# Optimization experiments

Measured on AMD Instinct MI355X. Metric: run time of the kernel, lower is better.

The kernel has to match this reference:

```python
import jax, jax.numpy as jnp
import numpy as np
from jax import lax

HID = 96              # hidden_dim (C)
DM  = 2 * HID         # SS2D d_model (real+imag interleaved channels)
DI  = 2 * DM          # d_inner (expand=2, VMamba default)
N   = 16              # d_state
K   = 4               # scan directions
R   = (DM + 15) // 16 # dt_rank = ceil(d_model/16)
B_, H_, W_ = 1, 64, 64


def _layernorm(x, w, b, eps=1e-5):
    m = x.mean(-1, keepdims=True)
    v = ((x - m) ** 2).mean(-1, keepdims=True)
    return (x - m) * lax.rsqrt(v + eps) * w + b


def _selective_scan(xs, delta, A, Bs, Cs):
    # xs, delta: (B,K,D,L); A: (K,D,N); Bs, Cs: (B,K,N,L)
    def step(h, inp):
        dt, Bt, Ct, ut = inp                              # (B,K,D),(B,K,N),(B,K,N),(B,K,D)
        dA = jnp.exp(dt[..., None] * A[None])             # (B,K,D,N)
        h = h * dA + dt[..., None] * Bt[:, :, None, :] * ut[..., None]
        y = jnp.einsum('bkdn,bkn->bkd', h, Ct)
        return h, y
    inputs = (jnp.moveaxis(delta, -1, 0), jnp.moveaxis(Bs, -1, 0),
              jnp.moveaxis(Cs, -1, 0), jnp.moveaxis(xs, -1, 0))
    h0 = jnp.zeros(xs.shape[:3] + (N,), xs.dtype)
    _, ys = lax.scan(step, h0, inputs)                    # (L,B,K,D)
    return jnp.moveaxis(ys, 0, -1)                        # (B,K,D,L)


def _forward_core(x, x_proj_w, dt_w, dt_b, A_logs, Ds):
    # x: (B, DI, H, W) -- 4-direction cross-scan (VMamba SS2D)
    B, D, H, W = x.shape
    L = H * W
    x_hw = x.reshape(B, D, L)
    x_wh = x.transpose(0, 1, 3, 2).reshape(B, D, L)
    x_hwwh = jnp.stack([x_hw, x_wh], axis=1)                    # (B,2,D,L)
    xs = jnp.concatenate([x_hwwh, jnp.flip(x_hwwh, -1)], 1)     # (B,4,D,L)
    x_dbl = jnp.einsum('bkdl,kcd->bkcl', xs, x_proj_w)          # (B,K,R+2N,L)
    dts, Bs, Cs = jnp.split(x_dbl, [R, R + N], axis=2)
    dts = jnp.einsum('bkrl,kdr->bkdl', dts, dt_w)
    delta = jax.nn.softplus(dts + dt_b[None, :, :, None])
    A = -jnp.exp(A_logs.reshape(K, D, N))
    ys = _selective_scan(xs, delta, A, Bs, Cs)
    out_y = ys + Ds.reshape(K, D)[None, :, :, None] * xs        # (B,4,D,L)
    inv_y = jnp.flip(out_y[:, 2:4], -1)
    tr = lambda t: t.reshape(B, D, W, H).transpose(0, 1, 3, 2).reshape(B, D, L)
    y = out_y[:, 0] + inv_y[:, 0] + tr(out_y[:, 1]) + tr(inv_y[:, 1])
    return y.transpose(0, 2, 1).reshape(B, H, W, D)


def _ss2d(x, in_proj_w, conv_w, conv_b, x_proj_w, dt_w, dt_b,
          A_logs, Ds, out_norm_w, out_norm_b, out_proj_w):
    # x: (B, H, Wf, DM)
    xz = x @ in_proj_w.T                                        # (B,H,Wf,2*DI)
    xc, z = jnp.split(xz, 2, axis=-1)
    xc = xc.transpose(0, 3, 1, 2)                               # (B,DI,H,Wf)
    xc = lax.conv_general_dilated(xc, conv_w, (1, 1), 'SAME',
                                  feature_group_count=DI,
                                  dimension_numbers=('NCHW', 'OIHW', 'NCHW'))
    xc = jax.nn.silu(xc + conv_b[None, :, None, None])
    y = _forward_core(xc, x_proj_w, dt_w, dt_b, A_logs, Ds)     # (B,H,Wf,DI)
    y = _layernorm(y, out_norm_w, out_norm_b)
    y = y * jax.nn.silu(z)
    return y @ out_proj_w.T                                     # (B,H,Wf,DM)


def _freq_vss(x, in_proj_w, conv_w, conv_b, x_proj_w, dt_w, dt_b,
              A_logs, Ds, out_norm_w, out_norm_b, out_proj_w):
    B, H, W, C = x.shape
    xf = jnp.fft.rfft2(x, axes=(1, 2), norm='ortho')            # (B,H,Wf,C) complex
    Wf = xf.shape[2]
    # interleave real/imag into channels: (B,H,Wf,C,2) -> (B,H,Wf,2C)
    x1 = jnp.stack([xf.real, xf.imag], axis=4).reshape(B, H, Wf, 2 * C)
    att = _ss2d(x1, in_proj_w, conv_w, conv_b, x_proj_w, dt_w, dt_b,
                A_logs, Ds, out_norm_w, out_norm_b, out_proj_w)
    att = att.reshape(B, H, Wf, C, 2)
    attc = lax.complex(att[..., 0], att[..., 1])
    x1r = jnp.fft.irfft2(attc, s=(H, W), axes=(1, 2), norm='ortho')
    return x + x1r                                              # residual (drop_path=0)


def setup_inputs() -> dict:
    key = jax.random.key(0)
    ks = jax.random.split(key, 8)
    s = 0.02
    return {
        'x': jax.random.normal(ks[0], (B_, H_, W_, HID), jnp.float32),
        'in_proj_w': jax.random.normal(ks[1], (2 * DI, DM), jnp.float32) * s,
        'conv_w': jax.random.normal(ks[2], (DI, 1, 3, 3), jnp.float32) * s,
        'conv_b': jnp.zeros((DI,), jnp.float32),
        'x_proj_w': jax.random.normal(ks[3], (K, R + 2 * N, DI), jnp.float32) * s,
        'dt_w': jax.random.normal(ks[4], (K, DI, R), jnp.float32) * s,
        'dt_b': jax.random.normal(ks[5], (K, DI), jnp.float32) * 0.1,
        'A_logs': jnp.tile(jnp.log(jnp.arange(1, N + 1, dtype=jnp.float32))[None], (K * DI, 1)),
        'Ds': jnp.ones((K * DI,), jnp.float32),
        'out_norm_w': jnp.ones((DI,), jnp.float32),
        'out_norm_b': jnp.zeros((DI,), jnp.float32),
        'out_proj_w': jax.random.normal(ks[6], (DM, DI), jnp.float32) * s,
    }


def reference(x, in_proj_w, conv_w, conv_b, x_proj_w, dt_w, dt_b,
              A_logs, Ds, out_norm_w, out_norm_b, out_proj_w):
    return _freq_vss(x, in_proj_w, conv_w, conv_b, x_proj_w, dt_w, dt_b,
                     A_logs, Ds, out_norm_w, out_norm_b, out_proj_w)
```

## Files before the change

### kernel.cpp

```cpp
#include <hip/hip_runtime.h>
#include <hip/hip_bf16.h>

#define LQ   2112
#define DQ   384
#define NST  16
#define HQ   64
#define WFQ  33
#define CQ   96
#define SC   33
#define KDN  24576

#define AIPW  0
#define ACW   147456
#define ACB   150912
#define AXPW  151296
#define ADTW  218880
#define ADTB  237312
#define AANEG 238848
#define ADS   263424
#define ANW   264960
#define ANB   265344
#define AOPW  265728
#define ARTOT 339456

#define OFF_FFT   339456
#define OFF_XZ    744960
#define OFF_XCV   2366976
#define OFF_G     3177984
#define OFF_SUMDT 3549696
#define OFF_HEND  3651072
#define OFF_YS    5273088

#define P_ZR  0
#define P_ZI  202752

static __device__ __forceinline__ float u2f(unsigned short u)
{ union { unsigned int i; float f; } v; v.i = ((unsigned int)u) << 16; return v.f; }

static __device__ __forceinline__ float ldin(const void* p, int o, int isbf)
{
    if (isbf) return u2f(((const unsigned short*)p)[o]);
    return ((const float*)p)[o];
}

static __device__ __forceinline__ int isbf_of(const void* ds)
{ return (((const unsigned int*)ds)[0] == 0x3F803F80u) ? 1 : 0; }

__global__ __launch_bounds__(256) void k_cvt_rfftw(
    const void* __restrict__ x,   const void* __restrict__ ipw,
    const void* __restrict__ cw,  const void* __restrict__ cb,
    const void* __restrict__ xpw, const void* __restrict__ dtw,
    const void* __restrict__ dtb, const void* __restrict__ alog,
    const void* __restrict__ ds,  const void* __restrict__ nw,
    const void* __restrict__ nb,  const void* __restrict__ opw,
    float* __restrict__ arena, float* __restrict__ Zr, float* __restrict__ Zi)
{
    const int isbf = isbf_of(ds);
    if (blockIdx.x < 1326) {
        int t = blockIdx.x * 256 + threadIdx.x;
        int o = t;
        if (o < 147456) { arena[t] = ldin(ipw, o, isbf); return; }  o -= 147456;
        if (o < 3456)   { arena[t] = ldin(cw, o, isbf);  return; }  o -= 3456;
        if (o < 384)    { arena[t] = ldin(cb, o, isbf);  return; }  o -= 384;
        if (o < 67584)  { arena[t] = ldin(xpw, o, isbf); return; }  o -= 67584;
        if (o < 18432)  { arena[t] = ldin(dtw, o, isbf); return; }  o -= 18432;
        if (o < 1536)   { arena[t] = ldin(dtb, o, isbf); return; }  o -= 1536;
        if (o < 24576)  { arena[t] = -expf(ldin(alog, o, isbf)); return; }  o -= 24576;
        if (o < 1536)   { arena[t] = ldin(ds, o, isbf);  return; }  o -= 1536;
        if (o < 384)    { arena[t] = ldin(nw, o, isbf);  return; }  o -= 384;
        if (o < 384)    { arena[t] = ldin(nb, o, isbf);  return; }  o -= 384;
        arena[t] = ldin(opw, o, isbf);
        return;
    }
    __shared__ float tc[64], ts[64];
    if (threadIdx.x < 64) {
        float ang = -6.283185307179586f * (float)threadIdx.x / 64.f;
        float s, c; __sincosf(ang, &s, &c); tc[threadIdx.x] = c; ts[threadIdx.x] = s;
    }
    __syncthreads();
    int tid = (blockIdx.x - 1326) * 256 + threadIdx.x;
    int c = tid % CQ; int f = (tid / CQ) % WFQ; int h = tid / (CQ * WFQ);
    const int base = h * 64 * CQ + c;
    float zr = 0.f, zi = 0.f; int j = 0;
#pragma unroll 4
    for (int w = 0; w < 64; w++) {
        float xv = ldin(x, base + w * CQ, isbf);
        zr += xv * tc[j]; zi += xv * ts[j];
        j += f; j &= 63;
    }
    Zr[tid] = zr; Zi[tid] = zi;
}

__global__ __launch_bounds__(256) void k_ffth(const float* __restrict__ Zr, const float* __restrict__ Zi,
                                              float* __restrict__ x1)
{
    __shared__ float tc[64], ts[64];
    if (threadIdx.x < 64) {
        float ang = -6.283185307179586f * (float)threadIdx.x / 64.f;
        float s, c; __sincosf(ang, &s, &c); tc[threadIdx.x] = c; ts[threadIdx.x] = s;
    }
    __syncthreads();
    int tid = blockIdx.x * 256 + threadIdx.x;
    int c = tid % CQ; int f = (tid / CQ) % WFQ; int u = tid / (CQ * WFQ);
    float xr = 0.f, xi = 0.f; int j = 0;
    int base = f * CQ + c;
#pragma unroll 4
    for (int h = 0; h < 64; h++) {
        float zr = Zr[base + h * (WFQ * CQ)];
        float zi = Zi[base + h * (WFQ * CQ)];
        xr += zr * tc[j] - zi * ts[j];
        xi += zr * ts[j] + zi * tc[j];
        j += u; j &= 63;
    }
    int l = u * WFQ + f;
    x1[l * 192 + 2 * c]     = xr * (1.f / 64.f);
    x1[l * 192 + 2 * c + 1] = xi * (1.f / 64.f);
}

typedef __attribute__((ext_vector_type(8))) __bf16 bf16x8;
typedef __attribute__((ext_vector_type(4))) float f32x4;

__global__ __launch_bounds__(256) void k_gemm(const float* __restrict__ A, const float* __restrict__ W,
                                              float* __restrict__ C, int N, int K, int sW, int sC)
{
    W += (size_t)blockIdx.z * sW; C += (size_t)blockIdx.z * sC;
    __shared__ __bf16 Asm[64 * 40];
    __shared__ __bf16 Bsm[64 * 40];
    const int tid = threadIdx.x;
    const int bm = blockIdx.y * 64, bn = blockIdx.x * 64;
    const int wv = tid >> 6, lane = tid & 63;
    const int srow = tid >> 2, skk = (tid & 3) * 8;
    const int fm = lane & 15, fq = lane >> 4;
    f32x4 acc0 = {0.f, 0.f, 0.f, 0.f}, acc1 = acc0, acc2 = acc0, acc3 = acc0;
    const __bf16* afp = Asm + (wv * 16 + fm) * 40 + fq * 8;
    const __bf16* bfp = Bsm + fm * 40 + fq * 8;
    for (int k0 = 0; k0 < K; k0 += 32) {
        {
            const float* ap = A + (size_t)(bm + srow) * K + k0 + skk;
            float4 a0 = *(const float4*)ap, a1 = *(const float4*)(ap + 4);
            bf16x8 v = { (__bf16)a0.x, (__bf16)a0.y, (__bf16)a0.z, (__bf16)a0.w,
                         (__bf16)a1.x, (__bf16)a1.y, (__bf16)a1.z, (__bf16)a1.w };
            *(bf16x8*)(Asm + srow * 40 + skk) = v;
        }
        {
            float4 b0 = {0.f,0.f,0.f,0.f}, b1 = b0;
            if (bn + srow < N) {
                const float* wp = W + (size_t)(bn + srow) * K + k0 + skk;
                b0 = *(const float4*)wp; b1 = *(const float4*)(wp + 4);
            }
            bf16x8 v = { (__bf16)b0.x, (__bf16)b0.y, (__bf16)b0.z, (__bf16)b0.w,
                         (__bf16)b1.x, (__bf16)b1.y, (__bf16)b1.z, (__bf16)b1.w };
            *(bf16x8*)(Bsm + srow * 40 + skk) = v;
        }
        __syncthreads();
        bf16x8 af = *(const bf16x8*)afp;
        bf16x8 fb0 = *(const bf16x8*)(bfp);
        bf16x8 fb1 = *(const bf16x8*)(bfp + 16 * 40);
        bf16x8 fb2 = *(const bf16x8*)(bfp + 32 * 40);
        bf16x8 fb3 = *(const bf16x8*)(bfp + 48 * 40);
        acc0 = __builtin_amdgcn_mfma_f32_16x16x32_bf16(af, fb0, acc0, 0, 0, 0);
        acc1 = __builtin_amdgcn_mfma_f32_16x16x32_bf16(af, fb1, acc1, 0, 0, 0);
        acc2 = __builtin_amdgcn_mfma_f32_16x16x32_bf16(af, fb2, acc2, 0, 0, 0);
        acc3 = __builtin_amdgcn_mfma_f32_16x16x32_bf16(af, fb3, acc3, 0, 0, 0);
        __syncthreads();
    }
    const int m0 = bm + wv * 16 + fq * 4;
#pragma unroll
    for (int nt = 0; nt < 4; nt++) {
        f32x4 a = (nt == 0) ? acc0 : ((nt == 1) ? acc1 : ((nt == 2) ? acc2 : acc3));
        int n = bn + nt * 16 + fm;
        if (n < N) {
#pragma unroll
            for (int r = 0; r < 4; r++)
                C[(size_t)(m0 + r) * N + n] = a[r];
        }
    }
}

__global__ __launch_bounds__(256) void k_conv(const float* __restrict__ xz,
                                              const float* __restrict__ ar,
                                              float* __restrict__ xcv)
{
    int tid = blockIdx.x * 256 + threadIdx.x;
    int d = tid % DQ; int lp = tid / DQ;
    int l0 = lp * 2;
    float w9[9];
#pragma unroll
    for (int i = 0; i < 9; i++) w9[i] = ar[ACW + d * 9 + i];
    float cb = ar[ACB + d];
#pragma unroll
    for (int q = 0; q < 2; q++) {
        int l = l0 + q;
        int h = l / WFQ; int f = l % WFQ;
        float acc = cb;
#pragma unroll
        for (int ky = 0; ky < 3; ky++) {
            int hh = h + ky - 1;
            if (hh < 0 || hh >= HQ) continue;
#pragma unroll
            for (int kx = 0; kx < 3; kx++) {
                int ff = f + kx - 1;
                if (ff < 0 || ff >= WFQ) continue;
                acc += w9[ky * 3 + kx] * xz[(size_t)(hh * WFQ + ff) * 768 + d];
            }
        }
        float sig = 1.f / (1.f + __expf(-acc));
        xcv[(size_t)l * DQ + d] = acc * sig;
    }
}

static __device__ __forceinline__ float softplus_f(float a)
{
    return (a > 15.f) ? a : __logf(1.f + __expf(a));
}

template<int KK> static __device__ __forceinline__ int chunk_l0(int s)
{
    if (KK == 0) return s * 64;
    if (KK == 1) return s;
    if (KK == 2) return 2111 - s * 64;
    return 2111 - s;
}
template<int KK> static __device__ __forceinline__ int chunk_stp()
{
    if (KK == 0) return 1;
    if (KK == 1) return 33;
    if (KK == 2) return -1;
    return -33;
}

template<int KK, int PASS2> static __device__ __forceinline__ void scan_body(
    const float* __restrict__ xcv, const float* __restrict__ G, const float* __restrict__ ar,
    float* __restrict__ hend, float* __restrict__ sumdt, float* __restrict__ ysum,
    float* __restrict__ dtL, float* __restrict__ duL)
{
    const int s = blockIdx.x, db = blockIdx.y;
    const int lane = threadIdx.x;
    const int d = lane & 15, ng = lane >> 4;
    const int stp = chunk_stp<KK>();
    const int l0 = chunk_l0<KK>(s);
    const float* Gk = G + (size_t)KK * (LQ * 44);

    {
        const int st = lane;
        const int lt = l0 + stp * st;
        const float* gr = Gk + lt * 44;
        float4 g0 = *(const float4*)(gr);
        float4 g1 = *(const float4*)(gr + 4);
        float4 g2 = *(const float4*)(gr + 8);
        const float* ub = xcv + (size_t)lt * DQ + db * 16;
        float uu[16];
        *(float4*)(uu)      = *(const float4*)(ub);
        *(float4*)(uu + 4)  = *(const float4*)(ub + 4);
        *(float4*)(uu + 8)  = *(const float4*)(ub + 8);
        *(float4*)(uu + 12) = *(const float4*)(ub + 12);
#pragma unroll
        for (int j = 0; j < 16; j++) {
            const int kdj = KK * DQ + db * 16 + j;
            const float* wp = ar + ADTW + kdj * 12;
            float acc = ar[ADTB + kdj]
                + wp[0] * g0.x + wp[1] * g0.y + wp[2]  * g0.z + wp[3]  * g0.w
                + wp[4] * g1.x + wp[5] * g1.y + wp[6]  * g1.z + wp[7]  * g1.w
                + wp[8] * g2.x + wp[9] * g2.y + wp[10] * g2.z + wp[11] * g2.w;
            float dtv = softplus_f(acc);
            dtL[st * 17 + j] = dtv;
            duL[st * 17 + j] = dtv * uu[j];
        }
    }
    if (!PASS2 && KK == 0) {
        float4 z4 = make_float4(0.f, 0.f, 0.f, 0.f);
        float* zp = ysum + (size_t)(l0 + lane) * DQ + db * 16;
        *(float4*)zp = z4; *(float4*)(zp + 4) = z4;
        *(float4*)(zp + 8) = z4; *(float4*)(zp + 12) = z4;
    }
    __syncthreads();

    const int kd = KK * DQ + db * 16 + d;
    const int kdn = kd * NST + 4 * ng;
    const float4 Av = *(const float4*)(ar + AANEG + kdn);
    float h0 = 0.f, h1 = 0.f, h2 = 0.f, h3 = 0.f;
    if (PASS2) {
        float4 hh = *(const float4*)(hend + (size_t)s * KDN + kdn);
        h0 = hh.x; h1 = hh.y; h2 = hh.z; h3 = hh.w;
    }

#pragma unroll 8
    for (int i = 0; i < 64; i++) {
        const int l = l0 + stp * i;
        float dt = dtL[i * 17 + d];
        float du = duL[i * 17 + d];
        float4 bv = *(const float4*)(Gk + l * 44 + 12 + 4 * ng);
        h0 = h0 * __expf(dt * Av.x) + du * bv.x;
        h1 = h1 * __expf(dt * Av.y) + du * bv.y;
        h2 = h2 * __expf(dt * Av.z) + du * bv.z;
        h3 = h3 * __expf(dt * Av.w) + du * bv.w;
        if (PASS2) {
            float4 cv = *(const float4*)(Gk + l * 44 + 28 + 4 * ng);
            float yp = h0 * cv.x + h1 * cv.y + h2 * cv.z + h3 * cv.w;
            yp += __shfl_xor(yp, 16);
            yp += __shfl_xor(yp, 32);
            if (ng == 0) atomicAdd(&ysum[(size_t)l * DQ + db * 16 + d], yp);
        }
    }

    if (!PASS2) {
        *(float4*)(hend + (size_t)s * KDN + kdn) = make_float4(h0, h1, h2, h3);
        float sd = 0.f;
#pragma unroll
        for (int t = 0; t < 16; t++) sd += dtL[(ng * 16 + t) * 17 + d];
        sd += __shfl_xor(sd, 16);
        sd += __shfl_xor(sd, 32);
        if (ng == 0) sumdt[s * 1536 + kd] = sd;
    }
}

__global__ __launch_bounds__(64, 4) void k_scan1(const float* __restrict__ xcv, const float* __restrict__ G,
                                                 const float* __restrict__ ar,
                                                 float* __restrict__ hend, float* __restrict__ sumdt,
                                                 float* __restrict__ ysum)
{
    __shared__ float smem[2 * 64 * 17];
    float* dtL = smem; float* duL = smem + 64 * 17;
    switch (blockIdx.z) {
        case 0: scan_body<0, 0>(xcv, G, ar, hend, sumdt, ysum, dtL, duL); break;
        case 1: scan_body<1, 0>(xcv, G, ar, hend, sumdt, ysum, dtL, duL); break;
        case 2: scan_body<2, 0>(xcv, G, ar, hend, sumdt, ysum, dtL, duL); break;
        default: scan_body<3, 0>(xcv, G, ar, hend, sumdt, ysum, dtL, duL); break;
    }
}

__global__ __launch_bounds__(64, 4) void k_scan2(const float* __restrict__ xcv, const float* __restrict__ G,
                                                 const float* __restrict__ ar,
                                                 float* __restrict__ hend, float* __restrict__ sumdt,
                                                 float* __restrict__ ysum)
{
    __shared__ float smem[2 * 64 * 17];
    float* dtL = smem; float* duL = smem + 64 * 17;
    switch (blockIdx.z) {
        case 0: scan_body<0, 1>(xcv, G, ar, hend, sumdt, ysum, dtL, duL); break;
        case 1: scan_body<1, 1>(xcv, G, ar, hend, sumdt, ysum, dtL, duL); break;
        case 2: scan_body<2, 1>(xcv, G, ar, hend, sumdt, ysum, dtL, duL); break;
        default: scan_body<3, 1>(xcv, G, ar, hend, sumdt, ysum, dtL, duL); break;
    }
}

__global__ __launch_bounds__(256) void k_comb(const float* __restrict__ ar, const float* __restrict__ sumdt,
                                              float* __restrict__ hend)
{
    int tid = blockIdx.x * 256 + threadIdx.x;
    int kd = tid >> 4;
    float Av = ar[AANEG + tid];
    float hp = 0.f;
    for (int s = 0; s < SC; s++) {
        float he = hend[(size_t)s * KDN + tid];
        hend[(size_t)s * KDN + tid] = hp;
        hp = hp * __expf(Av * sumdt[s * 1536 + kd]) + he;
    }
}

__global__ __launch_bounds__(256) void k_lngemm(const float* __restrict__ ysum, const float* __restrict__ xcv,
                                                const float* __restrict__ xz, const float* __restrict__ ar,
                                                float* __restrict__ att)
{
    __shared__ __bf16 Asm[64 * 40];
    __shared__ __bf16 Bsm[64 * 40];
    __shared__ float rowm[64], rowr[64];
    __shared__ float sdk[DQ], nwk[DQ], nbk[DQ];
    const int tid = threadIdx.x;
    const int bm = blockIdx.y * 64, bn = blockIdx.x * 64;

    for (int k = tid; k < DQ; k += 256) {
        sdk[k] = ar[ADS + k] + ar[ADS + DQ + k] + ar[ADS + 2 * DQ + k] + ar[ADS + 3 * DQ + k];
        nwk[k] = ar[ANW + k];
        nbk[k] = ar[ANB + k];
    }
    __syncthreads();

    {
        const int r = tid >> 2, seg = tid & 3;
        const float* yp = ysum + (size_t)(bm + r) * DQ + seg * 96;
        const float* xp = xcv  + (size_t)(bm + r) * DQ + seg * 96;
        float s1 = 0.f, s2 = 0.f;
#pragma unroll 8
        for (int k = 0; k < 96; k += 4) {
            float4 yv = *(const float4*)(yp + k);
            float4 xv = *(const float4*)(xp + k);
            float4 sv = *(const float4*)(sdk + seg * 96 + k);
            float a0 = yv.x + sv.x * xv.x; float a1 = yv.y + sv.y * xv.y;
            float a2 = yv.z + sv.z * xv.z; float a3 = yv.w + sv.w * xv.w;
            s1 += a0 + a1 + a2 + a3;
            s2 += a0 * a0 + a1 * a1 + a2 * a2 + a3 * a3;
        }
        s1 += __shfl_xor(s1, 1); s2 += __shfl_xor(s2, 1);
        s1 += __shfl_xor(s1, 2); s2 += __shfl_xor(s2, 2);
        if (seg == 0) {
            float m = s1 * (1.f / 384.f);
            float var = s2 * (1.f / 384.f) - m * m;
            rowm[r] = m; rowr[r] = rsqrtf(var + 1e-5f);
        }
    }
    __syncthreads();

    const int wv = tid >> 6, lane = tid & 63;
    const int srow = tid >> 2, skk = (tid & 3) * 8;
    const int fm = lane & 15, fq = lane >> 4;
    f32x4 acc0 = {0.f, 0.f, 0.f, 0.f}, acc1 = acc0, acc2 = acc0, acc3 = acc0;
    const __bf16* afp = Asm + (wv * 16 + fm) * 40 + fq * 8;
    const __bf16* bfp = Bsm + fm * 40 + fq * 8;
    const float W_rm = rowm[srow], W_rr = rowr[srow];
    for (int k0 = 0; k0 < 384; k0 += 32) {
        {
            const size_t rb = (size_t)(bm + srow) * DQ + k0 + skk;
            float4 y0 = *(const float4*)(ysum + rb), y1 = *(const float4*)(ysum + rb + 4);
            float4 x0 = *(const float4*)(xcv + rb),  x1 = *(const float4*)(xcv + rb + 4);
            const float* zp = xz + (size_t)(bm + srow) * 768 + 384 + k0 + skk;
            float4 z0 = *(const float4*)(zp), z1 = *(const float4*)(zp + 4);
            float va[8];
            float ya[8] = { y0.x, y0.y, y0.z, y0.w, y1.x, y1.y, y1.z, y1.w };
            float xa[8] = { x0.x, x0.y, x0.z, x0.w, x1.x, x1.y, x1.z, x1.w };
            float za[8] = { z0.x, z0.y, z0.z, z0.w, z1.x, z1.y, z1.z, z1.w };
#pragma unroll
            for (int e = 0; e < 8; e++) {
                int k = k0 + skk + e;
                float a = ya[e] + sdk[k] * xa[e];
                float zn = za[e];
                float sig = 1.f / (1.f + __expf(-zn));
                va[e] = ((a - W_rm) * W_rr * nwk[k] + nbk[k]) * (zn * sig);
            }
            bf16x8 v = { (__bf16)va[0], (__bf16)va[1], (__bf16)va[2], (__bf16)va[3],
                         (__bf16)va[4], (__bf16)va[5], (__bf16)va[6], (__bf16)va[7] };
            *(bf16x8*)(Asm + srow * 40 + skk) = v;
        }
        {
            const float* wp = ar + AOPW + (size_t)(bn + srow) * 384 + k0 + skk;
            float4 b0 = *(const float4*)wp, b1 = *(const float4*)(wp + 4);
            bf16x8 v = { (__bf16)b0.x, (__bf16)b0.y, (__bf16)b0.z, (__bf16)b0.w,
                         (__bf16)b1.x, (__bf16)b1.y, (__bf16)b1.z, (__bf16)b1.w };
            *(bf16x8*)(Bsm + srow * 40 + skk) = v;
        }
        __syncthreads();
        bf16x8 af = *(const bf16x8*)afp;
        bf16x8 fb0 = *(const bf16x8*)(bfp);
        bf16x8 fb1 = *(const bf16x8*)(bfp + 16 * 40);
        bf16x8 fb2 = *(const bf16x8*)(bfp + 32 * 40);
        bf16x8 fb3 = *(const bf16x8*)(bfp + 48 * 40);
        acc0 = __builtin_amdgcn_mfma_f32_16x16x32_bf16(af, fb0, acc0, 0, 0, 0);
        acc1 = __builtin_amdgcn_mfma_f32_16x16x32_bf16(af, fb1, acc1, 0, 0, 0);
        acc2 = __builtin_amdgcn_mfma_f32_16x16x32_bf16(af, fb2, acc2, 0, 0, 0);
        acc3 = __builtin_amdgcn_mfma_f32_16x16x32_bf16(af, fb3, acc3, 0, 0, 0);
        __syncthreads();
    }
    const int m0 = bm + wv * 16 + fq * 4;
#pragma unroll
    for (int nt = 0; nt < 4; nt++) {
        f32x4 a = (nt == 0) ? acc0 : ((nt == 1) ? acc1 : ((nt == 2) ? acc2 : acc3));
        int n = bn + nt * 16 + fm;
#pragma unroll
        for (int r = 0; r < 4; r++)
            att[(size_t)(m0 + r) * 192 + n] = a[r];
    }
}

__global__ __launch_bounds__(256) void k_iffth(const float* __restrict__ att,
                                               float* __restrict__ Yr, float* __restrict__ Yi)
{
    __shared__ float tc[64], ts[64];
    if (threadIdx.x < 64) {
        float ang = 6.283185307179586f * (float)threadIdx.x / 64.f;
        float s, c; __sincosf(ang, &s, &c); tc[threadIdx.x] = c; ts[threadIdx.x] = s;
    }
    __syncthreads();
    int tid = blockIdx.x * 256 + threadIdx.x;
    int c = tid % CQ; int f = (tid / CQ) % WFQ; int hp = tid / (CQ * WFQ);
    float yr = 0.f, yi = 0.f; int j = 0;
#pragma unroll 4
    for (int h = 0; h < 64; h++) {
        const float* ap = att + (size_t)(h * WFQ + f) * 192 + 2 * c;
        float arv = ap[0], aiv = ap[1];
        yr += arv * tc[j] - aiv * ts[j];
        yi += arv * ts[j] + aiv * tc[j];
        j += hp; j &= 63;
    }
    Yr[tid] = yr * 0.125f;
    Yi[tid] = yi * 0.125f;
}

__global__ __launch_bounds__(256) void k_irfft_res(const float* __restrict__ Yr, const float* __restrict__ Yi,
                                                   const void* __restrict__ x, const void* __restrict__ ds,
                                                   void* __restrict__ out)
{
    __shared__ float tc[64], ts[64];
    if (threadIdx.x < 64) {
        float ang = 6.283185307179586f * (float)threadIdx.x / 64.f;
        float s, c; __sincosf(ang, &s, &c); tc[threadIdx.x] = c; ts[threadIdx.x] = s;
    }
    __syncthreads();
    const int isbf = isbf_of(ds);
    int tid = blockIdx.x * 256 + threadIdx.x;
    int c = tid % CQ; int w = (tid / CQ) % 64; int h = tid / (CQ * 64);
    const float* yr = Yr + h * (WFQ * CQ) + c;
    const float* yi = Yi + h * (WFQ * CQ) + c;
    float acc = yr[0];
    acc += ((w & 1) ? -1.f : 1.f) * yr[32 * CQ];
    float a2 = 0.f; int j = w & 63;
#pragma unroll 4
    for (int f = 1; f < 32; f++) {
        a2 += yr[f * CQ] * tc[j] - yi[f * CQ] * ts[j];
        j += w; j &= 63;
    }
    acc += 2.f * a2;
    float val = ldin(x, tid, isbf) + 0.125f * acc;
    if (isbf) ((__hip_bfloat16*)out)[tid] = __float2bfloat16(val);
    else      ((float*)out)[tid] = val;
}

extern "C" void kernel_launch(void* const* d_in, const int* in_sizes, int n_in,
                              void* d_out, int out_size, void* d_ws, size_t ws_size,
                              hipStream_t stream)
{
    float* ws    = (float*)d_ws;
    float* ar    = ws;
    float* Zr    = ws + OFF_FFT + P_ZR;
    float* Zi    = ws + OFF_FFT + P_ZI;
    float* xz    = ws + OFF_XZ;
    float* xcv   = ws + OFF_XCV;
    float* G     = ws + OFF_G;
    float* sumdt = ws + OFF_SUMDT;
    float* hend  = ws + OFF_HEND;
    float* YS    = ws + OFF_YS;

    float* x1   = YS;
    float* ysum = YS;
    float* att  = hend;

    k_cvt_rfftw<<<2118, 256, 0, stream>>>(d_in[0], d_in[1], d_in[2], d_in[3], d_in[4], d_in[5],
                                          d_in[6], d_in[7], d_in[8], d_in[9], d_in[10], d_in[11],
                                          ar, Zr, Zi);
    k_ffth<<<792, 256, 0, stream>>>(Zr, Zi, x1);
    k_gemm<<<dim3(12, 33, 1), 256, 0, stream>>>(x1, ar + AIPW, xz, 768, 192, 0, 0);
    k_conv<<<1584, 256, 0, stream>>>(xz, ar, xcv);
    k_gemm<<<dim3(1, 33, 4), 256, 0, stream>>>(xcv, ar + AXPW, G, 44, 384, 44 * 384, LQ * 44);
    k_scan1<<<dim3(SC, 24, 4), 64, 0, stream>>>(xcv, G, ar, hend, sumdt, ysum);
    k_comb<<<96, 256, 0, stream>>>(ar, sumdt, hend);
    k_scan2<<<dim3(SC, 24, 4), 64, 0, stream>>>(xcv, G, ar, hend, sumdt, ysum);
    k_lngemm<<<dim3(3, 33, 1), 256, 0, stream>>>(ysum, xcv, xz, ar, att);
    k_iffth<<<792, 256, 0, stream>>>(att, Zr, Zi);
    k_irfft_res<<<1536, 256, 0, stream>>>(Zr, Zi, d_in[0], d_in[8], d_out);
}
```

Before: 226.7 us.

## Halve scan chunk length, stage B/C in LDS, batch y atomics, prefetch combine

Doubles the number of scan chunks from 33 to 66 so each chunk covers 32 steps, giving more parallel blocks and a shorter serial loop per block. The per-step B and C vectors are staged once in shared memory instead of being reloaded from global memory every step. Per-step y atomics are buffered in LDS and flushed in one pass at the end. The chunk-combine kernel now software-prefetches hend and sumdt in groups of six. The cost is a longer sequential combine pass, larger hend and sumdt buffers, and more shared memory per block.

```diff
diff --git a/kernel.cpp b/kernel.cpp
--- a/kernel.cpp
+++ b/kernel.cpp
@@ -7,7 +7,7 @@
 #define HQ   64
 #define WFQ  33
 #define CQ   96
-#define SC   33
+#define SC   66
 #define KDN  24576
 
 #define AIPW  0
@@ -216,10 +216,10 @@
 
 template<int KK> static __device__ __forceinline__ int chunk_l0(int s)
 {
-    if (KK == 0) return s * 64;
-    if (KK == 1) return s;
-    if (KK == 2) return 2111 - s * 64;
-    return 2111 - s;
+    if (KK == 0) return s * 32;
+    if (KK == 1) return (s & 1) * 1056 + (s >> 1);
+    if (KK == 2) return 2111 - s * 32;
+    return 2111 - (s & 1) * 1056 - (s >> 1);
 }
 template<int KK> static __device__ __forceinline__ int chunk_stp()
 {
@@ -232,7 +232,8 @@
 template<int KK, int PASS2> static __device__ __forceinline__ void scan_body(
     const float* __restrict__ xcv, const float* __restrict__ G, const float* __restrict__ ar,
     float* __restrict__ hend, float* __restrict__ sumdt, float* __restrict__ ysum,
-    float* __restrict__ dtL, float* __restrict__ duL)
+    float* __restrict__ dtL, float* __restrict__ duL,
+    float* __restrict__ bvL, float* __restrict__ cvL, float* __restrict__ yL)
 {
     const int s = blockIdx.x, db = blockIdx.y;
     const int lane = threadIdx.x;
@@ -242,32 +243,42 @@
     const float* Gk = G + (size_t)KK * (LQ * 44);
 
     {
-        const int st = lane;
+        const int st = lane & 31;
+        const int hi = lane >> 5;
+        const int jb = hi * 8;
         const int lt = l0 + stp * st;
         const float* gr = Gk + lt * 44;
         float4 g0 = *(const float4*)(gr);
         float4 g1 = *(const float4*)(gr + 4);
         float4 g2 = *(const float4*)(gr + 8);
-        const float* ub = xcv + (size_t)lt * DQ + db * 16;
-        float uu[16];
-        *(float4*)(uu)      = *(const float4*)(ub);
-        *(float4*)(uu + 4)  = *(const float4*)(ub + 4);
-        *(float4*)(uu + 8)  = *(const float4*)(ub + 8);
-        *(float4*)(uu + 12) = *(const float4*)(ub + 12);
-#pragma unroll
-        for (int j = 0; j < 16; j++) {
-            const int kdj = KK * DQ + db * 16 + j;
+        float4 b0 = *(const float4*)(gr + 12 + jb);
+        float4 b1 = *(const float4*)(gr + 16 + jb);
+        *(float4*)(bvL + st * 20 + jb)     = b0;
+        *(float4*)(bvL + st * 20 + jb + 4) = b1;
+        if (PASS2) {
+            float4 c0 = *(const float4*)(gr + 28 + jb);
+            float4 c1 = *(const float4*)(gr + 32 + jb);
+            *(float4*)(cvL + st * 20 + jb)     = c0;
+            *(float4*)(cvL + st * 20 + jb + 4) = c1;
+        }
+        const float* ub = xcv + (size_t)lt * DQ + db * 16 + jb;
+        float uu[8];
+        *(float4*)(uu)     = *(const float4*)(ub);
+        *(float4*)(uu + 4) = *(const float4*)(ub + 4);
+#pragma unroll
+        for (int j = 0; j < 8; j++) {
+            const int kdj = KK * DQ + db * 16 + jb + j;
             const float* wp = ar + ADTW + kdj * 12;
             float acc = ar[ADTB + kdj]
                 + wp[0] * g0.x + wp[1] * g0.y + wp[2]  * g0.z + wp[3]  * g0.w
                 + wp[4] * g1.x + wp[5] * g1.y + wp[6]  * g1.z + wp[7]  * g1.w
                 + wp[8] * g2.x + wp[9] * g2.y + wp[10] * g2.z + wp[11] * g2.w;
             float dtv = softplus_f(acc);
-            dtL[st * 17 + j] = dtv;
-            duL[st * 17 + j] = dtv * uu[j];
-        }
-    }
-    if (!PASS2 && KK == 0) {
+            dtL[st * 17 + jb + j] = dtv;
+            duL[st * 17 + jb + j] = dtv * uu[j];
+        }
+    }
+    if (!PASS2 && KK == 0 && lane < 32) {
         float4 z4 = make_float4(0.f, 0.f, 0.f, 0.f);
         float* zp = ysum + (size_t)(l0 + lane) * DQ + db * 16;
         *(float4*)zp = z4; *(float4*)(zp + 4) = z4;
@@ -285,21 +296,20 @@
     }
 
 #pragma unroll 8
-    for (int i = 0; i < 64; i++) {
-        const int l = l0 + stp * i;
+    for (int i = 0; i < 32; i++) {
         float dt = dtL[i * 17 + d];
         float du = duL[i * 17 + d];
-        float4 bv = *(const float4*)(Gk + l * 44 + 12 + 4 * ng);
+        float4 bv = *(const float4*)(bvL + i * 20 + 4 * ng);
         h0 = h0 * __expf(dt * Av.x) + du * bv.x;
         h1 = h1 * __expf(dt * Av.y) + du * bv.y;
         h2 = h2 * __expf(dt * Av.z) + du * bv.z;
         h3 = h3 * __expf(dt * Av.w) + du * bv.w;
         if (PASS2) {
-            float4 cv = *(const float4*)(Gk + l * 44 + 28 + 4 * ng);
+            float4 cv = *(const float4*)(cvL + i * 20 + 4 * ng);
             float yp = h0 * cv.x + h1 * cv.y + h2 * cv.z + h3 * cv.w;
             yp += __shfl_xor(yp, 16);
             yp += __shfl_xor(yp, 32);
-            if (ng == 0) atomicAdd(&ysum[(size_t)l * DQ + db * 16 + d], yp);
+            if (ng == 0) yL[i * 17 + d] = yp;
         }
     }
 
@@ -307,10 +317,18 @@
         *(float4*)(hend + (size_t)s * KDN + kdn) = make_float4(h0, h1, h2, h3);
         float sd = 0.f;
 #pragma unroll
-        for (int t = 0; t < 16; t++) sd += dtL[(ng * 16 + t) * 17 + d];
+        for (int t = 0; t < 8; t++) sd += dtL[(ng * 8 + t) * 17 + d];
         sd += __shfl_xor(sd, 16);
         sd += __shfl_xor(sd, 32);
         if (ng == 0) sumdt[s * 1536 + kd] = sd;
+    } else {
+        __syncthreads();
+        const int wst = lane & 31, whi = lane >> 5;
+        const int wl = l0 + stp * wst;
+        float* yp = ysum + (size_t)wl * DQ + db * 16 + whi * 8;
+#pragma unroll
+        for (int e = 0; e < 8; e++)
+            atomicAdd(yp + e, yL[wst * 17 + whi * 8 + e]);
     }
 }
 
@@ -319,13 +337,13 @@
                                                  float* __restrict__ hend, float* __restrict__ sumdt,
                                                  float* __restrict__ ysum)
 {
-    __shared__ float smem[2 * 64 * 17];
-    float* dtL = smem; float* duL = smem + 64 * 17;
+    __shared__ float smem[1728];
+    float* dtL = smem; float* duL = smem + 544; float* bvL = smem + 1088;
     switch (blockIdx.z) {
-        case 0: scan_body<0, 0>(xcv, G, ar, hend, sumdt, ysum, dtL, duL); break;
-        case 1: scan_body<1, 0>(xcv, G, ar, hend, sumdt, ysum, dtL, duL); break;
-        case 2: scan_body<2, 0>(xcv, G, ar, hend, sumdt, ysum, dtL, duL); break;
-        default: scan_body<3, 0>(xcv, G, ar, hend, sumdt, ysum, dtL, duL); break;
+        case 0: scan_body<0, 0>(xcv, G, ar, hend, sumdt, ysum, dtL, duL, bvL, nullptr, nullptr); break;
+        case 1: scan_body<1, 0>(xcv, G, ar, hend, sumdt, ysum, dtL, duL, bvL, nullptr, nullptr); break;
+        case 2: scan_body<2, 0>(xcv, G, ar, hend, sumdt, ysum, dtL, duL, bvL, nullptr, nullptr); break;
+        default: scan_body<3, 0>(xcv, G, ar, hend, sumdt, ysum, dtL, duL, bvL, nullptr, nullptr); break;
     }
 }
 
@@ -334,13 +352,14 @@
                                                  float* __restrict__ hend, float* __restrict__ sumdt,
                                                  float* __restrict__ ysum)
 {
-    __shared__ float smem[2 * 64 * 17];
-    float* dtL = smem; float* duL = smem + 64 * 17;
+    __shared__ float smem[2912];
+    float* dtL = smem; float* duL = smem + 544; float* bvL = smem + 1088;
+    float* cvL = smem + 1728; float* yL = smem + 2368;
     switch (blockIdx.z) {
-        case 0: scan_body<0, 1>(xcv, G, ar, hend, sumdt, ysum, dtL, duL); break;
-        case 1: scan_body<1, 1>(xcv, G, ar, hend, sumdt, ysum, dtL, duL); break;
-        case 2: scan_body<2, 1>(xcv, G, ar, hend, sumdt, ysum, dtL, duL); break;
-        default: scan_body<3, 1>(xcv, G, ar, hend, sumdt, ysum, dtL, duL); break;
+        case 0: scan_body<0, 1>(xcv, G, ar, hend, sumdt, ysum, dtL, duL, bvL, cvL, yL); break;
+        case 1: scan_body<1, 1>(xcv, G, ar, hend, sumdt, ysum, dtL, duL, bvL, cvL, yL); break;
+        case 2: scan_body<2, 1>(xcv, G, ar, hend, sumdt, ysum, dtL, duL, bvL, cvL, yL); break;
+        default: scan_body<3, 1>(xcv, G, ar, hend, sumdt, ysum, dtL, duL, bvL, cvL, yL); break;
     }
 }
 
@@ -350,11 +369,30 @@
     int tid = blockIdx.x * 256 + threadIdx.x;
     int kd = tid >> 4;
     float Av = ar[AANEG + tid];
+    float hbuf[6], sbuf[6];
+#pragma unroll
+    for (int q = 0; q < 6; q++) {
+        hbuf[q] = hend[(size_t)q * KDN + tid];
+        sbuf[q] = sumdt[q * 1536 + kd];
+    }
     float hp = 0.f;
-    for (int s = 0; s < SC; s++) {
-        float he = hend[(size_t)s * KDN + tid];
-        hend[(size_t)s * KDN + tid] = hp;
-        hp = hp * __expf(Av * sumdt[s * 1536 + kd]) + he;
+    for (int s = 0; s < SC; s += 6) {
+        float hc[6], sc6[6];
+#pragma unroll
+        for (int q = 0; q < 6; q++) { hc[q] = hbuf[q]; sc6[q] = sbuf[q]; }
+#pragma unroll
+        for (int q = 0; q < 6; q++) {
+            int sn = s + 6 + q;
+            if (sn < SC) {
+                hbuf[q] = hend[(size_t)sn * KDN + tid];
+                sbuf[q] = sumdt[sn * 1536 + kd];
+            }
+        }
+#pragma unroll
+        for (int q = 0; q < 6; q++) {
+            hend[(size_t)(s + q) * KDN + tid] = hp;
+            hp = hp * __expf(Av * sc6[q]) + hc[q];
+        }
     }
 }
 
```

New measurement: 283.2 us. 24.9% more time.
